# Kernel optimization log

Hardware: AMD Instinct MI355X
Metric: run time of the kernel (lower is better)

## Reference

```python
import jax, jax.numpy as jnp
import numpy as np

# Static config matching AdaConv(c_in=512, p=4, batch_size=8, s_d=512, c_out=512)
C_IN = 512
C_OUT = 512
N_GROUPS = 128  # c_in // p


def _conv(x, w, b, groups=1, padding='VALID'):
    # x: NCHW, w: OIHW
    y = jax.lax.conv_general_dilated(
        x, w, window_strides=(1, 1), padding=padding,
        dimension_numbers=('NCHW', 'OIHW', 'NCHW'),
        feature_group_count=groups)
    return y + b[None, :, None, None]


def setup_inputs() -> dict:
    key = jax.random.key(0)
    ks = jax.random.split(key, 9)
    f32 = jnp.float32
    s = 0.02  # small init scale to keep activations well-behaved
    inp = {
        'style_encoding': jax.random.normal(ks[0], (8, 512, 4, 4), f32),
        'predicted': jax.random.normal(ks[1], (8, 512, 64, 64), f32),
        'dw1_w': jax.random.normal(ks[2], (512, 512, 1, 1), f32) * s,
        'dw1_b': jnp.full((512,), 0.01, f32),
        'dw2_w': jax.random.normal(ks[3], (2048, 512, 2, 2), f32) * s,
        'dw2_b': jnp.full((2048,), 0.01, f32),
        'pk1_w': jax.random.normal(ks[4], (512, 512, 1, 1), f32) * s,
        'pk1_b': jnp.full((512,), 0.01, f32),
        'pk2_w': jax.random.normal(ks[5], (2048, 512, 1, 1), f32) * s,
        'pk2_b': jnp.full((2048,), 0.01, f32),
        'pb1_w': jax.random.normal(ks[6], (512, 512, 1, 1), f32) * s,
        'pb1_b': jnp.full((512,), 0.01, f32),
        'pb2_w': jax.random.normal(ks[7], (512, 512, 1, 1), f32) * s,
        'pb2_b': jnp.full((512,), 0.01, f32),
    }
    return inp


def reference(style_encoding, predicted,
              dw1_w, dw1_b, dw2_w, dw2_b,
              pk1_w, pk1_b, pk2_w, pk2_b,
              pb1_w, pb1_b, pb2_w, pb2_b):
    N = style_encoding.shape[0]
    lrelu = lambda x: jax.nn.leaky_relu(x, 0.01)

    # --- predict per-sample depthwise 3x3 kernels from style (4x4 -> 3x3) ---
    h = lrelu(_conv(style_encoding, dw1_w, dw1_b))           # [N, c_in, 4, 4]
    depthwise = _conv(h, dw2_w, dw2_b)                       # [N, c_out*(c_in/n_groups), 3, 3]
    depthwise = depthwise.reshape(N * C_OUT, C_IN // N_GROUPS, 3, 3)

    # --- predict per-sample pointwise kernels + bias from pooled style ---
    s_pool = jnp.mean(style_encoding, axis=(2, 3), keepdims=True)  # [N, s_d, 1, 1]
    pk = _conv(lrelu(_conv(s_pool, pk1_w, pk1_b)), pk2_w, pk2_b)
    pointwise_kn = pk.reshape(N * C_OUT, C_OUT // N_GROUPS, 1, 1)
    pb = _conv(lrelu(_conv(s_pool, pb1_w, pb1_b)), pb2_w, pb2_b)
    pointwise_bias = pb.reshape(N * C_OUT)

    # --- apply per-sample dynamic conv via huge-group grouped conv trick ---
    a, b, c, d = predicted.shape
    x = predicted.reshape(1, a * b, c, d)
    x = jnp.pad(x, ((0, 0), (0, 0), (1, 1), (1, 1)), mode='reflect')
    batch_groups = N * N_GROUPS
    y = jax.lax.conv_general_dilated(
        x, depthwise, (1, 1), 'VALID',
        dimension_numbers=('NCHW', 'OIHW', 'NCHW'),
        feature_group_count=batch_groups)                    # [1, N*c_out, c, d]
    y = jax.lax.conv_general_dilated(
        y, pointwise_kn, (1, 1), 'VALID',
        dimension_numbers=('NCHW', 'OIHW', 'NCHW'),
        feature_group_count=batch_groups)
    y = y + pointwise_bias[None, :, None, None]
    # permute([1,0,2,3]).view(a,b,c,d) with leading dim 1 == plain reshape
    return y.reshape(a, b, c, d)
```

## Files before the change

kernel.cpp:

```cpp
#include <hip/hip_runtime.h>

#define LRELU(x) ((x) > 0.f ? (x) : 0.01f * (x))

#define H2_OFF    0
#define T1_OFF    65536
#define T2_OFF    69632
#define PK_OFF    73728
#define PB_OFF    90112
#define WB_OFF    241664

__global__ __launch_bounds__(256) void kA(const float* __restrict__ style,
    const float* __restrict__ dw1_w, const float* __restrict__ dw1_b,
    const float* __restrict__ pk1_w, const float* __restrict__ pk1_b,
    const float* __restrict__ pb1_w, const float* __restrict__ pb1_b,
    float* __restrict__ h2t, float* __restrict__ t1, float* __restrict__ t2) {
  int b = blockIdx.x;
  int tid = threadIdx.x;
  __shared__ float smem[512];
  int wave = tid >> 6, l = tid & 63;
  float sv[8];
  if (b < 512) {
    int n = b >> 6; int pix = (b >> 2) & 15; int cq = b & 3;
    const float* sp = style + n * 8192 + pix;
#pragma unroll
    for (int j = 0; j < 8; ++j) sv[j] = sp[(8 * l + j) * 16];
    int cobase = cq * 128 + wave * 32;
    float res = (l < 32) ? dw1_b[cobase + l] : 0.f;
#pragma unroll 8
    for (int j = 0; j < 32; ++j) {
      const float4* wr = (const float4*)(dw1_w + (cobase + j) * 512 + 8 * l);
      float4 a = wr[0], c = wr[1];
      float v = a.x*sv[0] + a.y*sv[1] + a.z*sv[2] + a.w*sv[3]
              + c.x*sv[4] + c.y*sv[5] + c.z*sv[6] + c.w*sv[7];
      v += __shfl_xor(v, 1);
      v += __shfl_xor(v, 2);
      v += __shfl_xor(v, 4);
      v += __shfl_xor(v, 8);
      v += __shfl_xor(v, 16);
      v += __shfl_xor(v, 32);
      if (l == j) res += v;
    }
    if (l < 32) h2t[n * 8192 + (cobase + l) * 16 + pix] = LRELU(res);
  } else {
    int b2 = b - 512;
    int cq = b2 & 3; int which = (b2 >> 2) & 1; int n = b2 >> 3;
    for (int ci = tid; ci < 512; ci += 256) {
      const float4* r4 = (const float4*)(style + n * 8192 + ci * 16);
      float4 a = r4[0], bb = r4[1], c = r4[2], d = r4[3];
      smem[ci] = (a.x+a.y+a.z+a.w + bb.x+bb.y+bb.z+bb.w + c.x+c.y+c.z+c.w + d.x+d.y+d.z+d.w) * (1.f/16.f);
    }
    __syncthreads();
#pragma unroll
    for (int j = 0; j < 8; ++j) sv[j] = smem[8 * l + j];
    const float* w  = which ? pb1_w : pk1_w;
    const float* bv = which ? pb1_b : pk1_b;
    int cobase = cq * 128 + wave * 32;
    float* outp = (which ? t2 : t1) + n * 512;
    float res = (l < 32) ? bv[cobase + l] : 0.f;
#pragma unroll 8
    for (int j = 0; j < 32; ++j) {
      const float4* wr = (const float4*)(w + (cobase + j) * 512 + 8 * l);
      float4 a = wr[0], c = wr[1];
      float v = a.x*sv[0] + a.y*sv[1] + a.z*sv[2] + a.w*sv[3]
              + c.x*sv[4] + c.y*sv[5] + c.z*sv[6] + c.w*sv[7];
      v += __shfl_xor(v, 1);
      v += __shfl_xor(v, 2);
      v += __shfl_xor(v, 4);
      v += __shfl_xor(v, 8);
      v += __shfl_xor(v, 16);
      v += __shfl_xor(v, 32);
      if (l == j) res += v;
    }
    if (l < 32) outp[cobase + l] = LRELU(res);
  }
}

__global__ __launch_bounds__(256) void kB(const float* __restrict__ h2t,
    const float* __restrict__ dw2_w,
    const float* __restrict__ t1, const float* __restrict__ t2,
    const float* __restrict__ pk2_w, const float* __restrict__ pk2_b,
    const float* __restrict__ pb2_w, const float* __restrict__ pb2_b,
    float* __restrict__ PART, float* __restrict__ pk, float* __restrict__ pb) {
  __shared__ float smem[2592];
  int b = blockIdx.x;
  int tid = threadIdx.x;
  if (b < 512) {
    int bo = b & 15; int kc = b >> 4;
    float* ht = smem;
    {
      int f4 = tid * 2;
#pragma unroll
      for (int j = 0; j < 2; ++j) {
        int fi = f4 + j;
        int n = fi >> 6; int rem = fi & 63; int ci = rem >> 2; int q = rem & 3;
        float4 v = *(const float4*)(h2t + (size_t)n * 8192 + (kc * 16 + ci) * 16 + q * 4);
        *(float4*)&ht[n * 324 + ci * 20 + q * 4] = v;
      }
    }
    __syncthreads();
    int og = tid & 31; int n = tid >> 5;
    const float* hb = &ht[n * 324];
    int o2b = bo * 128 + og * 4;
    const float* wbase = dw2_w + (size_t)o2b * 2048 + kc * 64;
    float acc[9][4];
#pragma unroll
    for (int p = 0; p < 9; ++p)
#pragma unroll
      for (int oj = 0; oj < 4; ++oj) acc[p][oj] = 0.f;
#pragma unroll 2
    for (int ci = 0; ci < 16; ++ci) {
      const float* hr = hb + ci * 20;
      float4 a0 = *(const float4*)(hr);
      float4 a1 = *(const float4*)(hr + 4);
      float4 a2 = *(const float4*)(hr + 8);
      float4 a3 = *(const float4*)(hr + 12);
#pragma unroll
      for (int oj = 0; oj < 4; ++oj) {
        float4 w = *(const float4*)(wbase + (size_t)oj * 2048 + ci * 4);
        acc[0][oj] += w.x*a0.x + w.y*a0.y + w.z*a1.x + w.w*a1.y;
        acc[1][oj] += w.x*a0.y + w.y*a0.z + w.z*a1.y + w.w*a1.z;
        acc[2][oj] += w.x*a0.z + w.y*a0.w + w.z*a1.z + w.w*a1.w;
        acc[3][oj] += w.x*a1.x + w.y*a1.y + w.z*a2.x + w.w*a2.y;
        acc[4][oj] += w.x*a1.y + w.y*a1.z + w.z*a2.y + w.w*a2.z;
        acc[5][oj] += w.x*a1.z + w.y*a1.w + w.z*a2.z + w.w*a2.w;
        acc[6][oj] += w.x*a2.x + w.y*a2.y + w.z*a3.x + w.w*a3.y;
        acc[7][oj] += w.x*a2.y + w.y*a2.z + w.z*a3.y + w.w*a3.z;
        acc[8][oj] += w.x*a2.z + w.y*a2.w + w.z*a3.z + w.w*a3.w;
      }
    }
#pragma unroll
    for (int p = 0; p < 9; ++p) {
      float4 st; st.x = acc[p][0]; st.y = acc[p][1]; st.z = acc[p][2]; st.w = acc[p][3];
      *(float4*)&PART[(size_t)kc * 147456 + (size_t)(n * 9 + p) * 2048 + o2b] = st;
    }
  } else {
    int b2 = b - 512;
    int n = b2 / 20; int t20 = b2 % 20;
    bool isPb = t20 >= 16;
    int cobase = (isPb ? (t20 - 16) : t20) * 128;
    float* s = smem;
    const float* src = (isPb ? t2 : t1) + n * 512;
    for (int i = tid; i < 512; i += 256) s[i] = src[i];
    __syncthreads();
    int wave = tid >> 6, l = tid & 63;
    float sv[8];
#pragma unroll
    for (int j = 0; j < 8; ++j) sv[j] = s[8 * l + j];
    const float* w  = isPb ? pb2_w : pk2_w;
    const float* bv = isPb ? pb2_b : pk2_b;
    int cg = cobase + wave * 32;
    float res = (l < 32) ? bv[cg + l] : 0.f;
#pragma unroll 8
    for (int j = 0; j < 32; ++j) {
      const float4* wr = (const float4*)(w + (cg + j) * 512 + 8 * l);
      float4 a = wr[0], c = wr[1];
      float v = a.x*sv[0] + a.y*sv[1] + a.z*sv[2] + a.w*sv[3]
              + c.x*sv[4] + c.y*sv[5] + c.z*sv[6] + c.w*sv[7];
      v += __shfl_xor(v, 1);
      v += __shfl_xor(v, 2);
      v += __shfl_xor(v, 4);
      v += __shfl_xor(v, 8);
      v += __shfl_xor(v, 16);
      v += __shfl_xor(v, 32);
      if (l == j) res += v;
    }
    if (l < 32) {
      if (isPb) pb[n * 512 + cg + l] = res;
      else      pk[n * 2048 + cg + l] = res;
    }
  }
}

__global__ __launch_bounds__(256) void kW(const float* __restrict__ PART,
    const float* __restrict__ pk, const float* __restrict__ dw2_b,
    const float* __restrict__ pb, float* __restrict__ wbuf) {
  int idx = blockIdx.x * 256 + threadIdx.x;
  if (idx >= 8 * 128 * 160) return;
  int t = idx % 160; int Qn = idx / 160; int Q = Qn & 127; int n = Qn >> 7;
  if (t >= 144) {
    wbuf[idx] = (t < 148) ? pb[n * 512 + Q * 4 + (t - 144)] : 0.f;
    return;
  }
  int o = t & 3; int u = t >> 2; int kx = u % 3; int v = u / 3;
  int i = v & 3; int ky = v >> 2; int p = ky * 3 + kx;
  const float* pkp = pk + n * 2048 + 16 * Q + 4 * o;
  const float* bp  = dw2_b + 16 * Q;
  size_t dbase = (size_t)(n * 9 + p) * 2048 + 16 * Q;
  float sum = 0.f;
#pragma unroll
  for (int j = 0; j < 4; ++j) {
    float dv = bp[4 * j + i];
    size_t off = dbase + 4 * j + i;
#pragma unroll
    for (int s = 0; s < 32; ++s) dv += PART[(size_t)s * 147456 + off];
    sum += pkp[j] * dv;
  }
  wbuf[idx] = sum;
}

__global__ __launch_bounds__(256, 4) void kC(const float* __restrict__ x,
    const float* __restrict__ wbuf, float* __restrict__ out) {
  int b = blockIdx.x; int rt = b & 3; int Q = (b >> 2) & 127; int n = b >> 9;
  const float* wb = wbuf + (size_t)(n * 128 + Q) * 160;
  const float* base = x + (size_t)(n * 512 + Q * 4) * 4096;
  int e = threadIdx.x & 15;
  int y = rt * 16 + (threadIdx.x >> 4);
  int x0 = 4 * e;
  int ro[3];
#pragma unroll
  for (int ky = 0; ky < 3; ++ky) {
    int ry = y - 1 + ky;
    ry = ry < 0 ? 1 : (ry > 63 ? 62 : ry);
    ro[ky] = ry * 64;
  }
  float4 v[4][3];
#pragma unroll
  for (int i = 0; i < 4; ++i)
#pragma unroll
    for (int ky = 0; ky < 3; ++ky)
      v[i][ky] = *(const float4*)(base + i * 4096 + ro[ky] + x0);
  float acc[4][4];
#pragma unroll
  for (int o = 0; o < 4; ++o) {
    float bv = wb[144 + o];
#pragma unroll
    for (int px = 0; px < 4; ++px) acc[o][px] = bv;
  }
#pragma unroll
  for (int i = 0; i < 4; ++i) {
#pragma unroll
    for (int ky = 0; ky < 3; ++ky) {
      float vl = __shfl_up(v[i][ky].w, 1, 16);
      float vr = __shfl_down(v[i][ky].x, 1, 16);
      if (e == 0)  vl = v[i][ky].y;
      if (e == 15) vr = v[i][ky].z;
      float va0 = vl, va1 = v[i][ky].x, va2 = v[i][ky].y, va3 = v[i][ky].z,
            va4 = v[i][ky].w, va5 = vr;
#pragma unroll
      for (int kx = 0; kx < 3; ++kx) {
        const float* wp = &wb[((ky * 4 + i) * 3 + kx) * 4];
        float w0 = wp[0], w1 = wp[1], w2 = wp[2], w3 = wp[3];
        float xv0 = kx == 0 ? va0 : (kx == 1 ? va1 : va2);
        float xv1 = kx == 0 ? va1 : (kx == 1 ? va2 : va3);
        float xv2 = kx == 0 ? va2 : (kx == 1 ? va3 : va4);
        float xv3 = kx == 0 ? va3 : (kx == 1 ? va4 : va5);
        acc[0][0] += w0 * xv0; acc[0][1] += w0 * xv1; acc[0][2] += w0 * xv2; acc[0][3] += w0 * xv3;
        acc[1][0] += w1 * xv0; acc[1][1] += w1 * xv1; acc[1][2] += w1 * xv2; acc[1][3] += w1 * xv3;
        acc[2][0] += w2 * xv0; acc[2][1] += w2 * xv1; acc[2][2] += w2 * xv2; acc[2][3] += w2 * xv3;
        acc[3][0] += w3 * xv0; acc[3][1] += w3 * xv1; acc[3][2] += w3 * xv2; acc[3][3] += w3 * xv3;
      }
    }
  }
#pragma unroll
  for (int o = 0; o < 4; ++o) {
    float4 st; st.x = acc[o][0]; st.y = acc[o][1]; st.z = acc[o][2]; st.w = acc[o][3];
    *(float4*)&out[(((size_t)(n * 512 + Q * 4 + o)) * 64 + y) * 64 + x0] = st;
  }
}

extern "C" void kernel_launch(void* const* d_in, const int* in_sizes, int n_in,
                              void* d_out, int out_size, void* d_ws, size_t ws_size,
                              hipStream_t stream) {
  const float* style = (const float*)d_in[0];
  const float* pred  = (const float*)d_in[1];
  const float* dw1_w = (const float*)d_in[2];
  const float* dw1_b = (const float*)d_in[3];
  const float* dw2_w = (const float*)d_in[4];
  const float* dw2_b = (const float*)d_in[5];
  const float* pk1_w = (const float*)d_in[6];
  const float* pk1_b = (const float*)d_in[7];
  const float* pk2_w = (const float*)d_in[8];
  const float* pk2_b = (const float*)d_in[9];
  const float* pb1_w = (const float*)d_in[10];
  const float* pb1_b = (const float*)d_in[11];
  const float* pb2_w = (const float*)d_in[12];
  const float* pb2_b = (const float*)d_in[13];
  float* ws  = (float*)d_ws;
  float* h2t = ws + H2_OFF;
  float* t1  = ws + T1_OFF;
  float* t2  = ws + T2_OFF;
  float* pk  = ws + PK_OFF;
  float* pb  = ws + PB_OFF;
  float* wb  = ws + WB_OFF;
  float* out = (float*)d_out;
  float* PART = out;

  kA<<<576, 256, 0, stream>>>(style, dw1_w, dw1_b, pk1_w, pk1_b, pb1_w, pb1_b, h2t, t1, t2);
  kB<<<672, 256, 0, stream>>>(h2t, dw2_w, t1, t2, pk2_w, pk2_b, pb2_w, pb2_b, PART, pk, pb);
  kW<<<640, 256, 0, stream>>>(PART, pk, dw2_b, pb, wb);
  kC<<<4096, 256, 0, stream>>>(pred, wb, out);
}
```

Before: 74.60 us.

## Process all four row tiles per block in kC with double-buffered software pipelining

kC now launches one block per (sample, group) instead of four and loops over the four 16-row tiles. Loads for the next tile are issued into a second register buffer while the current tile is computed, with sched_barriers fixing that order. The intent is to hide global-load latency and reuse the per-group weights across tiles. In exchange it doubles the register footprint, drops the occupancy hint from 4 to 2 blocks per unit, and cuts the grid to 1024 blocks, which reduces the parallelism available to hide latency.

```diff
diff --git a/kernel.cpp b/kernel.cpp
--- a/kernel.cpp
+++ b/kernel.cpp
@@ -198,64 +198,82 @@
   wbuf[idx] = sum;
 }
 
-__global__ __launch_bounds__(256, 4) void kC(const float* __restrict__ x,
+__global__ __launch_bounds__(256, 2) void kC(const float* __restrict__ x,
     const float* __restrict__ wbuf, float* __restrict__ out) {
-  int b = blockIdx.x; int rt = b & 3; int Q = (b >> 2) & 127; int n = b >> 9;
+  int b = blockIdx.x; int Q = b & 127; int n = b >> 7;
   const float* wb = wbuf + (size_t)(n * 128 + Q) * 160;
   const float* base = x + (size_t)(n * 512 + Q * 4) * 4096;
   int e = threadIdx.x & 15;
-  int y = rt * 16 + (threadIdx.x >> 4);
+  int r = threadIdx.x >> 4;
   int x0 = 4 * e;
-  int ro[3];
-#pragma unroll
-  for (int ky = 0; ky < 3; ++ky) {
-    int ry = y - 1 + ky;
-    ry = ry < 0 ? 1 : (ry > 63 ? 62 : ry);
-    ro[ky] = ry * 64;
-  }
-  float4 v[4][3];
-#pragma unroll
-  for (int i = 0; i < 4; ++i)
-#pragma unroll
-    for (int ky = 0; ky < 3; ++ky)
-      v[i][ky] = *(const float4*)(base + i * 4096 + ro[ky] + x0);
-  float acc[4][4];
-#pragma unroll
-  for (int o = 0; o < 4; ++o) {
-    float bv = wb[144 + o];
-#pragma unroll
-    for (int px = 0; px < 4; ++px) acc[o][px] = bv;
-  }
-#pragma unroll
-  for (int i = 0; i < 4; ++i) {
+
+  auto ldG = [&](float4* d, int g) {
+    int y = g * 16 + r;
 #pragma unroll
     for (int ky = 0; ky < 3; ++ky) {
-      float vl = __shfl_up(v[i][ky].w, 1, 16);
-      float vr = __shfl_down(v[i][ky].x, 1, 16);
-      if (e == 0)  vl = v[i][ky].y;
-      if (e == 15) vr = v[i][ky].z;
-      float va0 = vl, va1 = v[i][ky].x, va2 = v[i][ky].y, va3 = v[i][ky].z,
-            va4 = v[i][ky].w, va5 = vr;
-#pragma unroll
-      for (int kx = 0; kx < 3; ++kx) {
-        const float* wp = &wb[((ky * 4 + i) * 3 + kx) * 4];
-        float w0 = wp[0], w1 = wp[1], w2 = wp[2], w3 = wp[3];
-        float xv0 = kx == 0 ? va0 : (kx == 1 ? va1 : va2);
-        float xv1 = kx == 0 ? va1 : (kx == 1 ? va2 : va3);
-        float xv2 = kx == 0 ? va2 : (kx == 1 ? va3 : va4);
-        float xv3 = kx == 0 ? va3 : (kx == 1 ? va4 : va5);
-        acc[0][0] += w0 * xv0; acc[0][1] += w0 * xv1; acc[0][2] += w0 * xv2; acc[0][3] += w0 * xv3;
-        acc[1][0] += w1 * xv0; acc[1][1] += w1 * xv1; acc[1][2] += w1 * xv2; acc[1][3] += w1 * xv3;
-        acc[2][0] += w2 * xv0; acc[2][1] += w2 * xv1; acc[2][2] += w2 * xv2; acc[2][3] += w2 * xv3;
-        acc[3][0] += w3 * xv0; acc[3][1] += w3 * xv1; acc[3][2] += w3 * xv2; acc[3][3] += w3 * xv3;
+      int ry = y - 1 + ky;
+      ry = ry < 0 ? 1 : (ry > 63 ? 62 : ry);
+#pragma unroll
+      for (int i = 0; i < 4; ++i)
+        d[i * 3 + ky] = *(const float4*)(base + i * 4096 + ry * 64 + x0);
+    }
+  };
+  auto cmpG = [&](const float4* v, int g) {
+    int y = g * 16 + r;
+    float acc[4][4];
+#pragma unroll
+    for (int o = 0; o < 4; ++o) {
+      float bv = wb[144 + o];
+#pragma unroll
+      for (int px = 0; px < 4; ++px) acc[o][px] = bv;
+    }
+#pragma unroll
+    for (int i = 0; i < 4; ++i) {
+#pragma unroll
+      for (int ky = 0; ky < 3; ++ky) {
+        float4 vv = v[i * 3 + ky];
+        float vl = __shfl_up(vv.w, 1, 16);
+        float vr = __shfl_down(vv.x, 1, 16);
+        if (e == 0)  vl = vv.y;
+        if (e == 15) vr = vv.z;
+        float va0 = vl, va1 = vv.x, va2 = vv.y, va3 = vv.z, va4 = vv.w, va5 = vr;
+#pragma unroll
+        for (int kx = 0; kx < 3; ++kx) {
+          const float* wp = &wb[((ky * 4 + i) * 3 + kx) * 4];
+          float w0 = wp[0], w1 = wp[1], w2 = wp[2], w3 = wp[3];
+          float xv0 = kx == 0 ? va0 : (kx == 1 ? va1 : va2);
+          float xv1 = kx == 0 ? va1 : (kx == 1 ? va2 : va3);
+          float xv2 = kx == 0 ? va2 : (kx == 1 ? va3 : va4);
+          float xv3 = kx == 0 ? va3 : (kx == 1 ? va4 : va5);
+          acc[0][0] += w0 * xv0; acc[0][1] += w0 * xv1; acc[0][2] += w0 * xv2; acc[0][3] += w0 * xv3;
+          acc[1][0] += w1 * xv0; acc[1][1] += w1 * xv1; acc[1][2] += w1 * xv2; acc[1][3] += w1 * xv3;
+          acc[2][0] += w2 * xv0; acc[2][1] += w2 * xv1; acc[2][2] += w2 * xv2; acc[2][3] += w2 * xv3;
+          acc[3][0] += w3 * xv0; acc[3][1] += w3 * xv1; acc[3][2] += w3 * xv2; acc[3][3] += w3 * xv3;
+        }
       }
     }
-  }
-#pragma unroll
-  for (int o = 0; o < 4; ++o) {
-    float4 st; st.x = acc[o][0]; st.y = acc[o][1]; st.z = acc[o][2]; st.w = acc[o][3];
-    *(float4*)&out[(((size_t)(n * 512 + Q * 4 + o)) * 64 + y) * 64 + x0] = st;
-  }
+#pragma unroll
+    for (int o = 0; o < 4; ++o) {
+      float4 st; st.x = acc[o][0]; st.y = acc[o][1]; st.z = acc[o][2]; st.w = acc[o][3];
+      *(float4*)&out[(((size_t)(n * 512 + Q * 4 + o)) * 64 + y) * 64 + x0] = st;
+    }
+  };
+
+  float4 A[12], B[12];
+  ldG(A, 0);
+  ldG(B, 1);
+  __builtin_amdgcn_sched_barrier(0);
+  cmpG(A, 0);
+  __builtin_amdgcn_sched_barrier(0);
+  ldG(A, 2);
+  __builtin_amdgcn_sched_barrier(0);
+  cmpG(B, 1);
+  __builtin_amdgcn_sched_barrier(0);
+  ldG(B, 3);
+  __builtin_amdgcn_sched_barrier(0);
+  cmpG(A, 2);
+  __builtin_amdgcn_sched_barrier(0);
+  cmpG(B, 3);
 }
 
 extern "C" void kernel_launch(void* const* d_in, const int* in_sizes, int n_in,
@@ -288,5 +306,5 @@
   kA<<<576, 256, 0, stream>>>(style, dw1_w, dw1_b, pk1_w, pk1_b, pb1_w, pb1_b, h2t, t1, t2);
   kB<<<672, 256, 0, stream>>>(h2t, dw2_w, t1, t2, pk2_w, pk2_b, pb2_w, pb2_b, PART, pk, pb);
   kW<<<640, 256, 0, stream>>>(PART, pk, dw2_b, pb, wb);
-  kC<<<4096, 256, 0, stream>>>(pred, wb, out);
-}
+  kC<<<1024, 256, 0, stream>>>(pred, wb, out);
+}
```

New measurement: 120.8 us. 1.62x slower.
